# Performance work log

Measured on AMD Instinct MI355X. Metric: run time of the kernel, lower is better.

## Reference

```python
import jax, jax.numpy as jnp
import numpy as np

N_NODES = 100000


def gcn_conv(x, W, b, src, dst, n_nodes):
    # PyG GCNConv: linear transform, add self-loops, symmetric normalization,
    # scatter-add aggregation from source to target, then bias.
    xl = x @ W  # [N, out]
    loops = jnp.arange(n_nodes, dtype=src.dtype)
    src2 = jnp.concatenate([src, loops])
    dst2 = jnp.concatenate([dst, loops])
    deg = jax.ops.segment_sum(jnp.ones_like(dst2, dtype=xl.dtype), dst2,
                              num_segments=n_nodes)
    dinv = jnp.where(deg > 0, jax.lax.rsqrt(deg), 0.0)
    norm = dinv[src2] * dinv[dst2]  # [E+N]
    msgs = norm[:, None] * xl[src2]  # gather + scale, [E+N, out]
    out = jax.ops.segment_sum(msgs, dst2, num_segments=n_nodes)
    return out + b


def setup_inputs() -> dict:
    key = jax.random.key(0)
    k1, k2, k3, k4, k5 = jax.random.split(key, 5)
    num_features, hidden, num_classes = 256, 64, 16
    x = jax.random.normal(k1, (N_NODES, num_features), dtype=jnp.float32)
    edge_index = jax.random.randint(k2, (2, 1600000), 0, N_NODES, dtype=jnp.int64)
    W1 = jax.random.normal(k3, (num_features, hidden), dtype=jnp.float32) / np.sqrt(num_features)
    b1 = jnp.zeros((hidden,), dtype=jnp.float32)
    W2 = jax.random.normal(k4, (hidden, num_classes), dtype=jnp.float32) / np.sqrt(hidden)
    b2 = jnp.zeros((num_classes,), dtype=jnp.float32)
    return {"x": x, "edge_index": edge_index, "W1": W1, "b1": b1,
            "W2": W2, "b2": b2}


def reference(x, edge_index, W1, b1, W2, b2):
    src, dst = edge_index[0], edge_index[1]
    h = gcn_conv(x, W1, b1, src, dst, N_NODES)
    h = jax.nn.relu(h)
    h = gcn_conv(h, W2, b2, src, dst, N_NODES)
    return jax.nn.log_softmax(h, axis=1)
```

## Files before the change

kernel.cpp:

```cpp
#include <hip/hip_runtime.h>
#include <hip/hip_bf16.h>


#define N_NODES 100000
#define BSH 7
#define BROW 128
#define NB ((N_NODES + BROW - 1) / BROW)
#define CAP 4096

__global__ __launch_bounds__(256) void k_bfill(const int* __restrict__ src,
                                               const int* __restrict__ dst, int E,
                                               int* __restrict__ gfill,
                                               int* __restrict__ bk) {
    __shared__ int cnt[NB];
    __shared__ int off[NB];
    __shared__ int cur[NB];
    int t = threadIdx.x;
    int chunk = (E + gridDim.x - 1) / gridDim.x;
    int e0 = blockIdx.x * chunk;
    int e1 = min(E, e0 + chunk);
    for (int b = t; b < NB; b += 256) { cnt[b] = 0; cur[b] = 0; }
    __syncthreads();
    for (int e = e0 + t; e < e1; e += 256)
        atomicAdd(&cnt[dst[e] >> BSH], 1);
    __syncthreads();
    for (int b = t; b < NB; b += 256)
        off[b] = cnt[b] ? atomicAdd(&gfill[b], cnt[b]) : 0;
    __syncthreads();
    for (int e = e0 + t; e < e1; e += 256) {
        int d = dst[e];
        int b = d >> BSH;
        int p = off[b] + atomicAdd(&cur[b], 1);
        if (p < CAP)
            bk[(size_t)b * CAP + p] = ((d & (BROW - 1)) << 17) | src[e];
    }
}

__global__ __launch_bounds__(1024) void k_scanN(const int* __restrict__ gfill,
                                                int* __restrict__ bbase) {
    __shared__ int s[1024];
    int t = threadIdx.x;
    int v = (t < NB) ? gfill[t] : 0;
    s[t] = v;
    __syncthreads();
    for (int off = 1; off < 1024; off <<= 1) {
        int a = (t >= off) ? s[t - off] : 0;
        __syncthreads();
        s[t] += a;
        __syncthreads();
    }
    if (t < NB) bbase[t] = s[t] - v;
}

__global__ __launch_bounds__(256) void k_bcsr(const int* __restrict__ gfill,
                                              const int* __restrict__ bbase,
                                              const int* __restrict__ bk,
                                              float* __restrict__ dinv,
                                              int* __restrict__ rowptr,
                                              int* __restrict__ csrc) {
    __shared__ int deg[BROW];
    __shared__ int pos[BROW];
    __shared__ int cur[BROW];
    int t = threadIdx.x;
    int b = blockIdx.x;
    if (t < BROW) deg[t] = 0;
    __syncthreads();
    int bn = min(gfill[b], CAP);
    const int* bp = bk + (size_t)b * CAP;
    for (int i = t; i < bn; i += 256)
        atomicAdd(&deg[bp[i] >> 17], 1);
    __syncthreads();
    if (t < BROW) pos[t] = deg[t];
    __syncthreads();
    for (int off = 1; off < BROW; off <<= 1) {
        int a = (t >= off && t < BROW) ? pos[t - off] : 0;
        __syncthreads();
        if (t < BROW) pos[t] += a;
        __syncthreads();
    }
    if (t < BROW) {
        int g = (b << BSH) + t;
        int gp = bbase[b] + pos[t] - deg[t];
        if (g <= N_NODES) rowptr[g] = gp;
        if (g < N_NODES) dinv[g] = rsqrtf((float)(deg[t] + 1));
        cur[t] = gp;
    }
    __syncthreads();
    for (int i = t; i < bn; i += 256) {
        int e = bp[i];
        int p = atomicAdd(&cur[e >> 17], 1);
        csrc[p] = e & 0x1FFFF;
    }
}


__global__ __launch_bounds__(256, 4) void k_gemm1(const float* __restrict__ x,
                                                  const float* __restrict__ W,
                                                  const float* __restrict__ dinv,
                                                  float* __restrict__ out, int n) {
    __shared__ float xtT[16 * 260];
    __shared__ float Wc[16 * 64];

    int t = threadIdx.x;
    int cg = t & 7;
    int rg = t >> 3;
    int rowBase = blockIdx.x * 256;

    float acc[8][8];
#pragma unroll
    for (int i = 0; i < 8; ++i)
#pragma unroll
        for (int j = 0; j < 8; ++j) acc[i][j] = 0.f;

    for (int kc = 0; kc < 256; kc += 16) {
        __syncthreads();
#pragma unroll
        for (int it = 0; it < 4; ++it) {
            int f4 = t + it * 256;
            int r  = f4 >> 2;
            int c4 = f4 & 3;
            float4 v = make_float4(0.f, 0.f, 0.f, 0.f);
            int gr = rowBase + r;
            if (gr < n)
                v = *reinterpret_cast<const float4*>(&x[(size_t)gr * 256 + kc + c4 * 4]);
            xtT[(c4 * 4 + 0) * 260 + r] = v.x;
            xtT[(c4 * 4 + 1) * 260 + r] = v.y;
            xtT[(c4 * 4 + 2) * 260 + r] = v.z;
            xtT[(c4 * 4 + 3) * 260 + r] = v.w;
        }
        reinterpret_cast<float4*>(Wc)[t] = reinterpret_cast<const float4*>(W)[kc * 16 + t];
        __syncthreads();
#pragma unroll
        for (int k = 0; k < 16; ++k) {
            float4 xa = *reinterpret_cast<const float4*>(&xtT[k * 260 + rg * 8]);
            float4 xb = *reinterpret_cast<const float4*>(&xtT[k * 260 + rg * 8 + 4]);
            float xv[8] = {xa.x, xa.y, xa.z, xa.w, xb.x, xb.y, xb.z, xb.w};
            float4 w0 = *reinterpret_cast<const float4*>(&Wc[k * 64 + cg * 8]);
            float4 w1 = *reinterpret_cast<const float4*>(&Wc[k * 64 + cg * 8 + 4]);
            float wv[8] = {w0.x, w0.y, w0.z, w0.w, w1.x, w1.y, w1.z, w1.w};
#pragma unroll
            for (int i = 0; i < 8; ++i)
#pragma unroll
                for (int j = 0; j < 8; ++j)
                    acc[i][j] = fmaf(xv[i], wv[j], acc[i][j]);
        }
    }

#pragma unroll
    for (int i = 0; i < 8; ++i) {
        int row = rowBase + rg * 8 + i;
        if (row < n) {
            float di = dinv[row];
            float* op = &out[(size_t)row * 64 + cg * 8];
            float4 v0 = {acc[i][0] * di, acc[i][1] * di, acc[i][2] * di, acc[i][3] * di};
            float4 v1 = {acc[i][4] * di, acc[i][5] * di, acc[i][6] * di, acc[i][7] * di};
            *reinterpret_cast<float4*>(op) = v0;
            *reinterpret_cast<float4*>(op + 4) = v1;
        }
    }
}

__global__ __launch_bounds__(256) void k_agg1(const float* __restrict__ xl,
                                              const int* __restrict__ rowptr,
                                              const int* __restrict__ csrc,
                                              const float* __restrict__ dinv,
                                              const float* __restrict__ b1,
                                              float* __restrict__ h, int n) {
    int t = threadIdx.x;
    int lane = t & 63;
    int node = blockIdx.x * 4 + (t >> 6);
    if (node >= n) return;
    float acc = xl[(size_t)node * 64 + lane];
    int p = rowptr[node], p1 = rowptr[node + 1];
    for (; p + 3 < p1; p += 4) {
        int s0 = csrc[p], s1 = csrc[p + 1], s2 = csrc[p + 2], s3 = csrc[p + 3];
        float v0 = xl[(size_t)s0 * 64 + lane];
        float v1 = xl[(size_t)s1 * 64 + lane];
        float v2 = xl[(size_t)s2 * 64 + lane];
        float v3 = xl[(size_t)s3 * 64 + lane];
        acc += v0; acc += v1; acc += v2; acc += v3;
    }
    for (; p < p1; ++p)
        acc += xl[(size_t)csrc[p] * 64 + lane];
    float o = fmaf(acc, dinv[node], b1[lane]);
    h[(size_t)node * 64 + lane] = fmaxf(o, 0.f);
}

__global__ __launch_bounds__(256) void k_gemm2(const float* __restrict__ h,
                                               const float* __restrict__ W,
                                               const float* __restrict__ dinv,
                                               float* __restrict__ out, int n) {
    int row = blockIdx.x * 256 + threadIdx.x;
    if (row >= n) return;
    float acc[16];
#pragma unroll
    for (int j = 0; j < 16; ++j) acc[j] = 0.f;
    const float* hr = &h[(size_t)row * 64];
#pragma unroll
    for (int k4 = 0; k4 < 16; ++k4) {
        float4 hv = *reinterpret_cast<const float4*>(&hr[k4 * 4]);
        float hvv[4] = {hv.x, hv.y, hv.z, hv.w};
#pragma unroll
        for (int kk = 0; kk < 4; ++kk) {
            const float* wr = &W[(size_t)(k4 * 4 + kk) * 16];
#pragma unroll
            for (int j = 0; j < 16; ++j) acc[j] = fmaf(hvv[kk], wr[j], acc[j]);
        }
    }
    float di = dinv[row];
    float* op = &out[(size_t)row * 16];
#pragma unroll
    for (int j = 0; j < 16; j += 4) {
        float4 v = {acc[j] * di, acc[j + 1] * di, acc[j + 2] * di, acc[j + 3] * di};
        *reinterpret_cast<float4*>(&op[j]) = v;
    }
}

__global__ __launch_bounds__(256) void k_agg2(const float* __restrict__ xl,
                                              const int* __restrict__ rowptr,
                                              const int* __restrict__ csrc,
                                              const float* __restrict__ dinv,
                                              const float* __restrict__ b2,
                                              float* __restrict__ out, int n) {
    int t = threadIdx.x;
    int l = t & 15;
    int node = blockIdx.x * 16 + (t >> 4);
    if (node >= n) return;
    float acc = xl[(size_t)node * 16 + l];
    int p = rowptr[node], p1 = rowptr[node + 1];
    for (; p + 1 < p1; p += 2) {
        int s0 = csrc[p], s1 = csrc[p + 1];
        float v0 = xl[(size_t)s0 * 16 + l];
        float v1 = xl[(size_t)s1 * 16 + l];
        acc += v0; acc += v1;
    }
    if (p < p1)
        acc += xl[(size_t)csrc[p] * 16 + l];
    float v = fmaf(acc, dinv[node], b2[l]);
    float mx = v;
#pragma unroll
    for (int o = 1; o < 16; o <<= 1) mx = fmaxf(mx, __shfl_xor(mx, o, 16));
    float ex = expf(v - mx);
    float ss = ex;
#pragma unroll
    for (int o = 1; o < 16; o <<= 1) ss += __shfl_xor(ss, o, 16);
    out[(size_t)node * 16 + l] = v - mx - logf(ss);
}


extern "C" void kernel_launch(void* const* d_in, const int* in_sizes, int n_in,
                              void* d_out, int out_size, void* d_ws, size_t ws_size,
                              hipStream_t stream) {
    const float* x  = (const float*)d_in[0];
    const int*   ei = (const int*)d_in[1];
    const float* W1 = (const float*)d_in[2];
    const float* b1 = (const float*)d_in[3];
    const float* W2 = (const float*)d_in[4];
    const float* b2 = (const float*)d_in[5];
    float* outp = (float*)d_out;

    const int n = N_NODES;
    const int E = in_sizes[1] / 2;
    const int* src = ei;
    const int* dst = ei + E;

    size_t off = 0;
    char* base = (char*)d_ws;
    auto take = [&](size_t bytes) { size_t r = off; off += (bytes + 255) & ~(size_t)255; return r; };
    int*   gfill  = (int*)(base + take((size_t)NB * 4));
    int*   bbase  = (int*)(base + take((size_t)NB * 4));
    int*   bk     = (int*)(base + take((size_t)NB * CAP * 4));
    float* dinv   = (float*)(base + take((size_t)n * 4));
    int*   rowptr = (int*)(base + take((size_t)(n + 1) * 4));
    int*   csrc   = (int*)(base + take((size_t)E * 4));
    float* xl1    = (float*)(base + take((size_t)n * 64 * 4));
    float* hbuf   = (float*)(base + take((size_t)n * 64 * 4));
    float* xl2    = (float*)(base + take((size_t)n * 16 * 4));

    hipMemsetAsync(gfill, 0, (size_t)NB * 4, stream);

    k_bfill<<<256, 256, 0, stream>>>(src, dst, E, gfill, bk);
    k_scanN<<<1, 1024, 0, stream>>>(gfill, bbase);
    k_bcsr<<<NB, 256, 0, stream>>>(gfill, bbase, bk, dinv, rowptr, csrc);

    k_gemm1<<<(n + 255) / 256, 256, 0, stream>>>(x, W1, dinv, xl1, n);
    k_agg1<<<(n + 3) / 4, 256, 0, stream>>>(xl1, rowptr, csrc, dinv, b1, hbuf, n);
    k_gemm2<<<(n + 255) / 256, 256, 0, stream>>>(hbuf, W2, dinv, xl2, n);
    k_agg2<<<(n + 15) / 16, 256, 0, stream>>>(xl2, rowptr, csrc, dinv, b2, outp, n);
}
```

Measured before the change: 386.2 us.

## Double-buffer GEMM1 shared tiles with register prefetch of next k-chunk

The first-layer GEMM now loads the next 16-wide k-chunk of x and W into registers while the current chunk is computed from shared memory, then writes it into a second shared buffer. This is meant to hide global-load latency behind the FMA loop. In exchange it doubles shared memory use, adds prefetch registers, and lowers the occupancy hint from 4 to 2 blocks per CU. There are still two barriers per chunk.

Result: slower. 661.0 us (+71.1%).

```diff
diff --git a/kernel.cpp b/kernel.cpp
--- a/kernel.cpp
+++ b/kernel.cpp
@@ -94,55 +94,83 @@
 }
 
 
-__global__ __launch_bounds__(256, 4) void k_gemm1(const float* __restrict__ x,
+__global__ __launch_bounds__(256, 2) void k_gemm1(const float* __restrict__ x,
                                                   const float* __restrict__ W,
                                                   const float* __restrict__ dinv,
                                                   float* __restrict__ out, int n) {
-    __shared__ float xtT[16 * 260];
-    __shared__ float Wc[16 * 64];
+    __shared__ float xtT[2][16 * 260];
+    __shared__ float Wc[2][16 * 64];
 
     int t = threadIdx.x;
     int cg = t & 7;
     int rg = t >> 3;
     int rowBase = blockIdx.x * 256;
 
-    float acc[8][8];
-#pragma unroll
-    for (int i = 0; i < 8; ++i)
-#pragma unroll
-        for (int j = 0; j < 8; ++j) acc[i][j] = 0.f;
-
-    for (int kc = 0; kc < 256; kc += 16) {
-        __syncthreads();
+    float4 xs[4];
+    float4 ws;
+
+    auto issue = [&](int chunk) {
+        int kc = chunk << 4;
 #pragma unroll
         for (int it = 0; it < 4; ++it) {
             int f4 = t + it * 256;
             int r  = f4 >> 2;
             int c4 = f4 & 3;
-            float4 v = make_float4(0.f, 0.f, 0.f, 0.f);
             int gr = rowBase + r;
+            xs[it] = make_float4(0.f, 0.f, 0.f, 0.f);
             if (gr < n)
-                v = *reinterpret_cast<const float4*>(&x[(size_t)gr * 256 + kc + c4 * 4]);
-            xtT[(c4 * 4 + 0) * 260 + r] = v.x;
-            xtT[(c4 * 4 + 1) * 260 + r] = v.y;
-            xtT[(c4 * 4 + 2) * 260 + r] = v.z;
-            xtT[(c4 * 4 + 3) * 260 + r] = v.w;
-        }
-        reinterpret_cast<float4*>(Wc)[t] = reinterpret_cast<const float4*>(W)[kc * 16 + t];
-        __syncthreads();
+                xs[it] = *reinterpret_cast<const float4*>(&x[(size_t)gr * 256 + kc + c4 * 4]);
+        }
+        ws = reinterpret_cast<const float4*>(W)[chunk * 256 + t];
+    };
+    auto commit = [&](int buf) {
+#pragma unroll
+        for (int it = 0; it < 4; ++it) {
+            int f4 = t + it * 256;
+            int r  = f4 >> 2;
+            int c4 = f4 & 3;
+            float* dp = &xtT[buf][0];
+            dp[(c4 * 4 + 0) * 260 + r] = xs[it].x;
+            dp[(c4 * 4 + 1) * 260 + r] = xs[it].y;
+            dp[(c4 * 4 + 2) * 260 + r] = xs[it].z;
+            dp[(c4 * 4 + 3) * 260 + r] = xs[it].w;
+        }
+        reinterpret_cast<float4*>(&Wc[buf][0])[t] = ws;
+    };
+
+    float acc[8][8];
+#pragma unroll
+    for (int i = 0; i < 8; ++i)
+#pragma unroll
+        for (int j = 0; j < 8; ++j) acc[i][j] = 0.f;
+
+    issue(0);
+    commit(0);
+    __syncthreads();
+
+    for (int c = 0; c < 16; ++c) {
+        int cur = c & 1;
+        if (c < 15) issue(c + 1);
+        const float* xp = &xtT[cur][0];
+        const float* wp = &Wc[cur][0];
 #pragma unroll
         for (int k = 0; k < 16; ++k) {
-            float4 xa = *reinterpret_cast<const float4*>(&xtT[k * 260 + rg * 8]);
-            float4 xb = *reinterpret_cast<const float4*>(&xtT[k * 260 + rg * 8 + 4]);
+            float4 xa = *reinterpret_cast<const float4*>(&xp[k * 260 + rg * 8]);
+            float4 xb = *reinterpret_cast<const float4*>(&xp[k * 260 + rg * 8 + 4]);
             float xv[8] = {xa.x, xa.y, xa.z, xa.w, xb.x, xb.y, xb.z, xb.w};
-            float4 w0 = *reinterpret_cast<const float4*>(&Wc[k * 64 + cg * 8]);
-            float4 w1 = *reinterpret_cast<const float4*>(&Wc[k * 64 + cg * 8 + 4]);
+            float4 w0 = *reinterpret_cast<const float4*>(&wp[k * 64 + cg * 8]);
+            float4 w1 = *reinterpret_cast<const float4*>(&wp[k * 64 + cg * 8 + 4]);
             float wv[8] = {w0.x, w0.y, w0.z, w0.w, w1.x, w1.y, w1.z, w1.w};
 #pragma unroll
             for (int i = 0; i < 8; ++i)
 #pragma unroll
                 for (int j = 0; j < 8; ++j)
                     acc[i][j] = fmaf(xv[i], wv[j], acc[i][j]);
+        }
+        if (c < 15) {
+            __syncthreads();
+            commit(cur ^ 1);
+            __syncthreads();
         }
     }
 
```
